# Performance work log

Hardware: AMD Instinct MI355X
Metric: run time of the kernel (lower is better)

## Reference

```python
import math
import jax, jax.numpy as jnp
import numpy as np

B, S, D, H = 4, 2048, 1024, 16
DH = D // H  # 64


def setup_inputs() -> dict:
    key = jax.random.key(0)
    k1, k2, k3 = jax.random.split(key, 3)
    x = jax.random.normal(k1, (B, S, D), dtype=jnp.float32)
    W_qkv = jax.random.normal(k2, (D, 3 * D), dtype=jnp.float32) * (1.0 / math.sqrt(D))
    b_qkv = jax.random.normal(k3, (3 * D,), dtype=jnp.float32) * 0.02
    return {"x": x, "W_qkv": W_qkv, "b_qkv": b_qkv}


def reference(x, W_qkv, b_qkv):
    b, s, d = x.shape
    qkv = x @ W_qkv + b_qkv                       # [B,S,3D]
    # Faithful to torch: view(B,S,H,3,D_h) -> interleaved per-head q/k/v split
    qkv = qkv.reshape(b, s, H, 3, DH)
    q = jnp.transpose(qkv[:, :, :, 0, :], (0, 2, 1, 3))  # [B,H,S,DH]
    k = jnp.transpose(qkv[:, :, :, 1, :], (0, 2, 1, 3))
    v = jnp.transpose(qkv[:, :, :, 2, :], (0, 2, 1, 3))
    scores = jnp.einsum('bhsd,bhtd->bhst', q, k) / math.sqrt(DH)  # [B,H,S,S]
    causal = jnp.triu(jnp.ones((s, s), dtype=bool), k=1)
    scores = jnp.where(causal, -jnp.inf, scores)
    weights = jax.nn.softmax(scores, axis=-1)
    # dropout is identity in eval/reference mode
    context = jnp.einsum('bhst,bhtd->bhsd', weights, v)  # [B,H,S,DH]
    return jnp.transpose(context, (0, 2, 1, 3)).reshape(b, s, d)
```

## Files before the change

### kernel.cpp

```cpp
#include <hip/hip_runtime.h>
#include <hip/hip_bf16.h>

#define Bz 4
#define Sz 2048
#define Dz 1024
#define Hz 16
#define DHz 64
#define Mz (Bz*Sz)
#define N3z (3*Dz)
#define Kz Dz

typedef short s16x8 __attribute__((ext_vector_type(8)));
typedef float f32x4 __attribute__((ext_vector_type(4)));
typedef unsigned short u16;

__device__ __forceinline__ u16 f2b(float f) {
  union { float f; unsigned u; } v; v.f = f;
  unsigned r = v.u + 0x7FFFu + ((v.u >> 16) & 1u);
  return (u16)(r >> 16);
}

__global__ __launch_bounds__(256) void cvt_x(const float* __restrict__ x,
                                             u16* __restrict__ xb) {
  int i = (blockIdx.x * 256 + threadIdx.x) * 4;
  float4 v = *reinterpret_cast<const float4*>(x + i);
  ushort4 o;
  o.x = f2b(v.x); o.y = f2b(v.y); o.z = f2b(v.z); o.w = f2b(v.w);
  *reinterpret_cast<ushort4*>(xb + i) = o;
}

__global__ __launch_bounds__(256) void transpose_w(const float* __restrict__ W,
                                                   u16* __restrict__ Wt) {
  __shared__ u16 t[32][33];
  int nb = blockIdx.x;
  int kb = blockIdx.y;
  int tx = threadIdx.x, ty = threadIdx.y;
#pragma unroll
  for (int j = 0; j < 4; ++j) {
    int k = kb * 32 + ty + j * 8;
    t[ty + j * 8][tx] = f2b(W[(size_t)k * N3z + nb * 32 + tx]);
  }
  __syncthreads();
#pragma unroll
  for (int j = 0; j < 4; ++j) {
    int n = nb * 32 + ty + j * 8;
    Wt[(size_t)n * Kz + kb * 32 + tx] = t[tx][ty + j * 8];
  }
}

#define BM 128
#define BN 128
#define BKs 32

__global__ __launch_bounds__(256) void qkv_gemm(
    const u16* __restrict__ A, const u16* __restrict__ Bt,
    const float* __restrict__ bias,
    u16* __restrict__ Qo, u16* __restrict__ Ko, u16* __restrict__ Vo) {
  __shared__ alignas(16) u16 As[BM * BKs];
  __shared__ alignas(16) u16 Bs[BN * BKs];
  const int tid = threadIdx.x;
  const int wid = tid >> 6, lane = tid & 63;
  const int wr = wid >> 1, wc = wid & 1;
  const int g = lane >> 4, lq = lane & 15;
  const int brow = blockIdx.x * BM;
  const int bcol = blockIdx.y * BN;

  f32x4 acc[4][4] = {};

  for (int kt = 0; kt < Kz; kt += BKs) {
#pragma unroll
    for (int c = 0; c < 2; ++c) {
      int row = (wid * 2 + c) * 16 + (lane >> 2);
      int off = (lane & 3) * 8;
      const u16* ga = A + (size_t)(brow + row) * Kz + kt + off;
      __builtin_amdgcn_global_load_lds(
          (const __attribute__((address_space(1))) void*)ga,
          (__attribute__((address_space(3))) void*)&As[(wid * 2 + c) * 512],
          16, 0, 0);
      const u16* gb = Bt + (size_t)(bcol + row) * Kz + kt + off;
      __builtin_amdgcn_global_load_lds(
          (const __attribute__((address_space(1))) void*)gb,
          (__attribute__((address_space(3))) void*)&Bs[(wid * 2 + c) * 512],
          16, 0, 0);
    }
    __syncthreads();

    s16x8 af[4], bfr[4];
#pragma unroll
    for (int i = 0; i < 4; ++i) {
      af[i]  = *reinterpret_cast<const s16x8*>(&As[(wr * 64 + i * 16 + lq) * BKs + g * 8]);
      bfr[i] = *reinterpret_cast<const s16x8*>(&Bs[(wc * 64 + i * 16 + lq) * BKs + g * 8]);
    }
#pragma unroll
    for (int mi = 0; mi < 4; ++mi)
#pragma unroll
      for (int ni = 0; ni < 4; ++ni)
        acc[mi][ni] = __builtin_amdgcn_mfma_f32_16x16x32_bf16(af[mi], bfr[ni], acc[mi][ni], 0, 0, 0);
    __syncthreads();
  }

#pragma unroll
  for (int ni = 0; ni < 4; ++ni) {
    int gcol = bcol + wc * 64 + ni * 16 + lq;
    int h = gcol / 192;
    int rem = gcol - h * 192;
    int tt = rem >> 6;
    int dh = rem & 63;
    float bv = bias[gcol];
    u16* dst = (tt == 0) ? Qo : (tt == 1) ? Ko : Vo;
    float scale = (tt == 0) ? 0.125f : 1.0f;
#pragma unroll
    for (int mi = 0; mi < 4; ++mi) {
#pragma unroll
      for (int r = 0; r < 4; ++r) {
        int grow = brow + wr * 64 + mi * 16 + g * 4 + r;
        int bb = grow >> 11;
        int ss = grow & 2047;
        float v = (acc[mi][ni][r] + bv) * scale;
        dst[(((size_t)bb * Hz + h) * Sz + ss) * DHz + dh] = f2b(v);
      }
    }
  }
}

#define PSTR 72

__global__ __launch_bounds__(512, 4) void attn_kernel(
    const u16* __restrict__ Qg, const u16* __restrict__ Kg,
    const u16* __restrict__ Vg, float* __restrict__ out) {
  __shared__ alignas(16) u16 Ks[64 * 64];
  __shared__ alignas(16) u16 Vs[64 * 64];
  __shared__ alignas(16) u16 Ps[8][16 * PSTR];

  const int qpair = blockIdx.x;
  const int bh = blockIdx.y;
  const int tid = threadIdx.x;
  const int wid = tid >> 6, lane = tid & 63;
  const int g = lane >> 4, lq = lane & 15;
  const size_t base = (size_t)bh * Sz * DHz;
  const int b = bh >> 4, h = bh & 15;

  const int krow = tid >> 3;
  const int kslot = tid & 7;
  const int kswz = kslot ^ (krow & 7);
  const int vkey = tid & 63;
  const int vdh0 = (tid >> 6) * 8;

  char* KsB = (char*)Ks;
  char* VsB = (char*)Vs;

  for (int half = 0; half < 2; ++half) {
    const int qt = half ? (15 - qpair) : qpair;
    const int q0w = qt * 128 + wid * 16;

    s16x8 qf0 = *reinterpret_cast<const s16x8*>(Qg + base + (size_t)(q0w + lq) * DHz + g * 8);
    s16x8 qf1 = *reinterpret_cast<const s16x8*>(Qg + base + (size_t)(q0w + lq) * DHz + g * 8 + 32);

    f32x4 o[4] = {};
    float m[4] = {-1e30f, -1e30f, -1e30f, -1e30f};
    float l[4] = {0.f, 0.f, 0.f, 0.f};

    const int nt = 2 * qt + 2;
    for (int t = 0; t < nt; ++t) {
      const int kv0 = t * 64;

      s16x8 kvv = *reinterpret_cast<const s16x8*>(Kg + base + (size_t)(kv0 + krow) * DHz + kslot * 8);
      *reinterpret_cast<s16x8*>(KsB + krow * 128 + kswz * 16) = kvv;
      s16x8 vvv = *reinterpret_cast<const s16x8*>(Vg + base + (size_t)(kv0 + vkey) * DHz + vdh0);
#pragma unroll
      for (int j = 0; j < 8; ++j) {
        int byte = (vdh0 + j) * 128 + vkey * 2;
        byte ^= (j << 4);
        *reinterpret_cast<u16*>(VsB + byte) = (u16)vvv[j];
      }
      __syncthreads();

      const bool active = (kv0 <= q0w + 15);
      if (active) {
        f32x4 sc[4];
#pragma unroll
        for (int f = 0; f < 4; ++f) {
          int row = f * 16 + lq;
          s16x8 kb0 = *reinterpret_cast<const s16x8*>(KsB + row * 128 + ((g ^ (row & 7)) << 4));
          s16x8 kb1 = *reinterpret_cast<const s16x8*>(KsB + row * 128 + (((g + 4) ^ (row & 7)) << 4));
          f32x4 z = {0.f, 0.f, 0.f, 0.f};
          z = __builtin_amdgcn_mfma_f32_16x16x32_bf16(qf0, kb0, z, 0, 0, 0);
          z = __builtin_amdgcn_mfma_f32_16x16x32_bf16(qf1, kb1, z, 0, 0, 0);
          sc[f] = z;
        }

        if (kv0 + 63 > q0w) {
#pragma unroll
          for (int f = 0; f < 4; ++f)
#pragma unroll
            for (int r = 0; r < 4; ++r) {
              int key = kv0 + f * 16 + lq;
              int q = q0w + g * 4 + r;
              if (key > q) sc[f][r] = -1e30f;
            }
        }

        float alpha[4];
#pragma unroll
        for (int r = 0; r < 4; ++r) {
          float v = fmaxf(fmaxf(sc[0][r], sc[1][r]), fmaxf(sc[2][r], sc[3][r]));
          v = fmaxf(v, __shfl_xor(v, 1));
          v = fmaxf(v, __shfl_xor(v, 2));
          v = fmaxf(v, __shfl_xor(v, 4));
          v = fmaxf(v, __shfl_xor(v, 8));
          float mn = fmaxf(m[r], v);
          alpha[r] = __expf(m[r] - mn);
          m[r] = mn;
        }
#pragma unroll
        for (int f = 0; f < 4; ++f)
#pragma unroll
          for (int r = 0; r < 4; ++r)
            sc[f][r] = __expf(sc[f][r] - m[r]);
#pragma unroll
        for (int r = 0; r < 4; ++r) {
          float s = sc[0][r] + sc[1][r] + sc[2][r] + sc[3][r];
          s += __shfl_xor(s, 1);
          s += __shfl_xor(s, 2);
          s += __shfl_xor(s, 4);
          s += __shfl_xor(s, 8);
          l[r] = l[r] * alpha[r] + s;
          o[0][r] *= alpha[r]; o[1][r] *= alpha[r];
          o[2][r] *= alpha[r]; o[3][r] *= alpha[r];
        }

#pragma unroll
        for (int f = 0; f < 4; ++f)
#pragma unroll
          for (int r = 0; r < 4; ++r)
            Ps[wid][(g * 4 + r) * PSTR + f * 16 + lq] = f2b(sc[f][r]);

        s16x8 pa0 = *reinterpret_cast<const s16x8*>(&Ps[wid][lq * PSTR + g * 8]);
        s16x8 pa1 = *reinterpret_cast<const s16x8*>(&Ps[wid][lq * PSTR + g * 8 + 32]);
#pragma unroll
        for (int ni = 0; ni < 4; ++ni) {
          int row = ni * 16 + lq;
          s16x8 vb0 = *reinterpret_cast<const s16x8*>(VsB + row * 128 + ((g ^ (row & 7)) << 4));
          s16x8 vb1 = *reinterpret_cast<const s16x8*>(VsB + row * 128 + (((g + 4) ^ (row & 7)) << 4));
          o[ni] = __builtin_amdgcn_mfma_f32_16x16x32_bf16(pa0, vb0, o[ni], 0, 0, 0);
          o[ni] = __builtin_amdgcn_mfma_f32_16x16x32_bf16(pa1, vb1, o[ni], 0, 0, 0);
        }
      }
      __syncthreads();
    }

#pragma unroll
    for (int r = 0; r < 4; ++r) {
      float inv = 1.0f / l[r];
      int s = q0w + g * 4 + r;
      float* op = out + (((size_t)b * Sz + s) * Hz + h) * DHz;
#pragma unroll
      for (int ni = 0; ni < 4; ++ni)
        op[ni * 16 + lq] = o[ni][r] * inv;
    }
  }
}

extern "C" void kernel_launch(void* const* d_in, const int* in_sizes, int n_in,
                              void* d_out, int out_size, void* d_ws, size_t ws_size,
                              hipStream_t stream) {
  const float* x    = (const float*)d_in[0];
  const float* W    = (const float*)d_in[1];
  const float* bias = (const float*)d_in[2];
  float* out = (float*)d_out;

  char* ws = (char*)d_ws;
  u16* xb = (u16*)(ws);
  u16* wt = (u16*)(ws + 16777216);
  u16* Qb = (u16*)(ws + 23068672);
  u16* Kb = (u16*)(ws + 39845888);
  u16* Vb = (u16*)(ws + 56623104);

  cvt_x<<<8192, 256, 0, stream>>>(x, xb);
  transpose_w<<<dim3(96, 32), dim3(32, 8), 0, stream>>>(W, wt);
  qkv_gemm<<<dim3(Mz / BM, N3z / BN), 256, 0, stream>>>(xb, wt, bias, Qb, Kb, Vb);
  attn_kernel<<<dim3(8, Bz * Hz), 512, 0, stream>>>(Qb, Kb, Vb, out);
}
```

Baseline: 262.2 us.

## Compute transposed scores in registers, use exp2 softmax with lazy rescaling

Swaps the MFMA operands so each lane holds a single query row's scores, which shrinks the row max and sum reductions to two cross-lane shuffles. The log2(e) factor is folded into the Q scale so the softmax can use exp2, and the running max is only updated when it grows by more than 8 (in log2 units). P is packed to bf16 with v_cvt_pk_bf16 and rearranged with shuffles instead of going through the per-warp LDS buffer. This removes LDS traffic and reduction work from the attention loop, at the cost of more complex lane permutation logic and looser numerical bounds on the unnormalised probabilities.

```diff
diff --git a/kernel.cpp b/kernel.cpp
--- a/kernel.cpp
+++ b/kernel.cpp
@@ -20,6 +20,12 @@
   return (u16)(r >> 16);
 }
 
+__device__ __forceinline__ unsigned cvt_pk_bf16(float lo, float hi) {
+  unsigned r;
+  asm("v_cvt_pk_bf16_f32 %0, %1, %2" : "=v"(r) : "v"(lo), "v"(hi));
+  return r;
+}
+
 __global__ __launch_bounds__(256) void cvt_x(const float* __restrict__ x,
                                              u16* __restrict__ xb) {
   int i = (blockIdx.x * 256 + threadIdx.x) * 4;
@@ -51,6 +57,7 @@
 #define BM 128
 #define BN 128
 #define BKs 32
+#define QSCALE (0.125f * 1.44269504088896f)
 
 __global__ __launch_bounds__(256) void qkv_gemm(
     const u16* __restrict__ A, const u16* __restrict__ Bt,
@@ -108,7 +115,7 @@
     int dh = rem & 63;
     float bv = bias[gcol];
     u16* dst = (tt == 0) ? Qo : (tt == 1) ? Ko : Vo;
-    float scale = (tt == 0) ? 0.125f : 1.0f;
+    float scale = (tt == 0) ? QSCALE : 1.0f;
 #pragma unroll
     for (int mi = 0; mi < 4; ++mi) {
 #pragma unroll
@@ -123,14 +130,11 @@
   }
 }
 
-#define PSTR 72
-
 __global__ __launch_bounds__(512, 4) void attn_kernel(
     const u16* __restrict__ Qg, const u16* __restrict__ Kg,
     const u16* __restrict__ Vg, float* __restrict__ out) {
   __shared__ alignas(16) u16 Ks[64 * 64];
   __shared__ alignas(16) u16 Vs[64 * 64];
-  __shared__ alignas(16) u16 Ps[8][16 * PSTR];
 
   const int qpair = blockIdx.x;
   const int bh = blockIdx.y;
@@ -149,16 +153,24 @@
   char* KsB = (char*)Ks;
   char* VsB = (char*)Vs;
 
+  const int p = g & 1;
+  const int cb = g >> 1;
+  const int sA = 32 * (g & 1) + lq;
+  const int sB = sA + 16;
+  const int sEven = cb ? sB : sA;
+  const int sOdd  = cb ? sA : sB;
+
   for (int half = 0; half < 2; ++half) {
     const int qt = half ? (15 - qpair) : qpair;
     const int q0w = qt * 128 + wid * 16;
+    const int qrow = q0w + lq;
 
     s16x8 qf0 = *reinterpret_cast<const s16x8*>(Qg + base + (size_t)(q0w + lq) * DHz + g * 8);
     s16x8 qf1 = *reinterpret_cast<const s16x8*>(Qg + base + (size_t)(q0w + lq) * DHz + g * 8 + 32);
 
     f32x4 o[4] = {};
-    float m[4] = {-1e30f, -1e30f, -1e30f, -1e30f};
-    float l[4] = {0.f, 0.f, 0.f, 0.f};
+    float m1 = -1e30f;
+    float l1 = 0.f;
 
     const int nt = 2 * qt + 2;
     for (int t = 0; t < nt; ++t) {
@@ -177,16 +189,16 @@
 
       const bool active = (kv0 <= q0w + 15);
       if (active) {
-        f32x4 sc[4];
+        f32x4 z[4];
 #pragma unroll
         for (int f = 0; f < 4; ++f) {
           int row = f * 16 + lq;
           s16x8 kb0 = *reinterpret_cast<const s16x8*>(KsB + row * 128 + ((g ^ (row & 7)) << 4));
           s16x8 kb1 = *reinterpret_cast<const s16x8*>(KsB + row * 128 + (((g + 4) ^ (row & 7)) << 4));
-          f32x4 z = {0.f, 0.f, 0.f, 0.f};
-          z = __builtin_amdgcn_mfma_f32_16x16x32_bf16(qf0, kb0, z, 0, 0, 0);
-          z = __builtin_amdgcn_mfma_f32_16x16x32_bf16(qf1, kb1, z, 0, 0, 0);
-          sc[f] = z;
+          f32x4 zz = {0.f, 0.f, 0.f, 0.f};
+          zz = __builtin_amdgcn_mfma_f32_16x16x32_bf16(kb0, qf0, zz, 0, 0, 0);
+          zz = __builtin_amdgcn_mfma_f32_16x16x32_bf16(kb1, qf1, zz, 0, 0, 0);
+          z[f] = zz;
         }
 
         if (kv0 + 63 > q0w) {
@@ -194,69 +206,92 @@
           for (int f = 0; f < 4; ++f)
 #pragma unroll
             for (int r = 0; r < 4; ++r) {
-              int key = kv0 + f * 16 + lq;
-              int q = q0w + g * 4 + r;
-              if (key > q) sc[f][r] = -1e30f;
+              int key = kv0 + f * 16 + g * 4 + r;
+              if (key > qrow) z[f][r] = -1e30f;
             }
         }
 
-        float alpha[4];
-#pragma unroll
-        for (int r = 0; r < 4; ++r) {
-          float v = fmaxf(fmaxf(sc[0][r], sc[1][r]), fmaxf(sc[2][r], sc[3][r]));
-          v = fmaxf(v, __shfl_xor(v, 1));
-          v = fmaxf(v, __shfl_xor(v, 2));
-          v = fmaxf(v, __shfl_xor(v, 4));
-          v = fmaxf(v, __shfl_xor(v, 8));
-          float mn = fmaxf(m[r], v);
-          alpha[r] = __expf(m[r] - mn);
-          m[r] = mn;
-        }
+        float pm = z[0][0];
 #pragma unroll
         for (int f = 0; f < 4; ++f)
 #pragma unroll
-          for (int r = 0; r < 4; ++r)
-            sc[f][r] = __expf(sc[f][r] - m[r]);
-#pragma unroll
-        for (int r = 0; r < 4; ++r) {
-          float s = sc[0][r] + sc[1][r] + sc[2][r] + sc[3][r];
-          s += __shfl_xor(s, 1);
-          s += __shfl_xor(s, 2);
-          s += __shfl_xor(s, 4);
-          s += __shfl_xor(s, 8);
-          l[r] = l[r] * alpha[r] + s;
-          o[0][r] *= alpha[r]; o[1][r] *= alpha[r];
-          o[2][r] *= alpha[r]; o[3][r] *= alpha[r];
-        }
-
-#pragma unroll
-        for (int f = 0; f < 4; ++f)
-#pragma unroll
-          for (int r = 0; r < 4; ++r)
-            Ps[wid][(g * 4 + r) * PSTR + f * 16 + lq] = f2b(sc[f][r]);
-
-        s16x8 pa0 = *reinterpret_cast<const s16x8*>(&Ps[wid][lq * PSTR + g * 8]);
-        s16x8 pa1 = *reinterpret_cast<const s16x8*>(&Ps[wid][lq * PSTR + g * 8 + 32]);
+          for (int r = 0; r < 4; ++r) pm = fmaxf(pm, z[f][r]);
+        pm = fmaxf(pm, __shfl_xor(pm, 16));
+        pm = fmaxf(pm, __shfl_xor(pm, 32));
+
+        if (!__all(pm <= m1 + 8.0f)) {
+          float mn = fmaxf(m1, pm);
+          float a = exp2f(m1 - mn);
+          m1 = mn;
+          l1 *= a;
+          float a0 = __shfl(a, 4 * g + 0);
+          float a1 = __shfl(a, 4 * g + 1);
+          float a2 = __shfl(a, 4 * g + 2);
+          float a3 = __shfl(a, 4 * g + 3);
+#pragma unroll
+          for (int ni = 0; ni < 4; ++ni) {
+            o[ni][0] *= a0; o[ni][1] *= a1; o[ni][2] *= a2; o[ni][3] *= a3;
+          }
+        }
+
+        float s = 0.f;
+        unsigned w[4][2];
+#pragma unroll
+        for (int f = 0; f < 4; ++f) {
+          float p0 = exp2f(z[f][0] - m1);
+          float p1 = exp2f(z[f][1] - m1);
+          float p2 = exp2f(z[f][2] - m1);
+          float p3 = exp2f(z[f][3] - m1);
+          s += (p0 + p1) + (p2 + p3);
+          w[f][0] = cvt_pk_bf16(p0, p1);
+          w[f][1] = cvt_pk_bf16(p2, p3);
+        }
+        s += __shfl_xor(s, 16);
+        s += __shfl_xor(s, 32);
+        l1 += s;
+
+        int e0 = __shfl((int)(p ? w[1][0] : w[0][0]), sEven);
+        int o0 = __shfl((int)(p ? w[0][0] : w[1][0]), sOdd);
+        int e1 = __shfl((int)(p ? w[1][1] : w[0][1]), sEven);
+        int o1 = __shfl((int)(p ? w[0][1] : w[1][1]), sOdd);
+        int e2 = __shfl((int)(p ? w[3][0] : w[2][0]), sEven);
+        int o2 = __shfl((int)(p ? w[2][0] : w[3][0]), sOdd);
+        int e3 = __shfl((int)(p ? w[3][1] : w[2][1]), sEven);
+        int o3 = __shfl((int)(p ? w[2][1] : w[3][1]), sOdd);
+        union { int i[4]; s16x8 v; } A0, A1;
+        A0.i[0] = cb ? o0 : e0;
+        A0.i[2] = cb ? e0 : o0;
+        A0.i[1] = cb ? o1 : e1;
+        A0.i[3] = cb ? e1 : o1;
+        A1.i[0] = cb ? o2 : e2;
+        A1.i[2] = cb ? e2 : o2;
+        A1.i[1] = cb ? o3 : e3;
+        A1.i[3] = cb ? e3 : o3;
+
 #pragma unroll
         for (int ni = 0; ni < 4; ++ni) {
           int row = ni * 16 + lq;
           s16x8 vb0 = *reinterpret_cast<const s16x8*>(VsB + row * 128 + ((g ^ (row & 7)) << 4));
           s16x8 vb1 = *reinterpret_cast<const s16x8*>(VsB + row * 128 + (((g + 4) ^ (row & 7)) << 4));
-          o[ni] = __builtin_amdgcn_mfma_f32_16x16x32_bf16(pa0, vb0, o[ni], 0, 0, 0);
-          o[ni] = __builtin_amdgcn_mfma_f32_16x16x32_bf16(pa1, vb1, o[ni], 0, 0, 0);
+          o[ni] = __builtin_amdgcn_mfma_f32_16x16x32_bf16(A0.v, vb0, o[ni], 0, 0, 0);
+          o[ni] = __builtin_amdgcn_mfma_f32_16x16x32_bf16(A1.v, vb1, o[ni], 0, 0, 0);
         }
       }
       __syncthreads();
     }
 
+    float lr0 = __shfl(l1, 4 * g + 0);
+    float lr1 = __shfl(l1, 4 * g + 1);
+    float lr2 = __shfl(l1, 4 * g + 2);
+    float lr3 = __shfl(l1, 4 * g + 3);
+    float inv[4] = {1.0f / lr0, 1.0f / lr1, 1.0f / lr2, 1.0f / lr3};
 #pragma unroll
     for (int r = 0; r < 4; ++r) {
-      float inv = 1.0f / l[r];
       int s = q0w + g * 4 + r;
       float* op = out + (((size_t)b * Sz + s) * Hz + h) * DHz;
 #pragma unroll
       for (int ni = 0; ni < 4; ++ni)
-        op[ni * 16 + lq] = o[ni][r] * inv;
+        op[ni * 16 + lq] = o[ni][r] * inv[r];
     }
   }
 }
```

Result: faster. 233.5 us (-10.9%).
